# Kernel tuning notes

Hardware: AMD Instinct MI355X
Metric: run time of the kernel (lower is better)

## Reference

```python
import jax, jax.numpy as jnp
import numpy as np

C = 64          # channels
HEADS = 4       # num_heads -> head_dim = 16
HID = int(C * 2.66)  # 170, GDFN hidden channels
B, H, W = 2, 256, 256


def conv1x1(x, w):
    # x: (b,c,h,w), w: (o,c) -> pointwise conv, no bias
    return jnp.einsum('bchw,oc->bohw', x, w)


def dwconv3x3(x, w):
    # depthwise 3x3, SAME padding; w: (C,1,3,3)
    return jax.lax.conv_general_dilated(
        x, w, window_strides=(1, 1), padding='SAME',
        feature_group_count=x.shape[1],
        dimension_numbers=('NCHW', 'OIHW', 'NCHW'))


def layer_norm_c(x, w, b):
    # torch: LayerNorm over channel dim of (b, hw, c), eps=1e-5
    mu = x.mean(axis=1, keepdims=True)
    var = ((x - mu) ** 2).mean(axis=1, keepdims=True)
    xn = (x - mu) / jnp.sqrt(var + 1e-5)
    return xn * w[None, :, None, None] + b[None, :, None, None]


def l2norm(x):
    # F.normalize(dim=-1), eps=1e-12
    n = jnp.sqrt(jnp.sum(x * x, axis=-1, keepdims=True))
    return x / jnp.maximum(n, 1e-12)


def mdta(x, temp, w_qkv, w_qkv_dw, w_po, w_kv, w_kv_dw, w_pof):
    b, c, h, w_ = x.shape
    d = c // HEADS
    qkv = dwconv3x3(conv1x1(x, w_qkv), w_qkv_dw)
    q, k, v = jnp.split(qkv, 3, axis=1)
    rs = lambda t: t.reshape(b, HEADS, d, h * w_)
    q, k, v = l2norm(rs(q)), l2norm(rs(k)), rs(v)
    # channel attention: (b,heads,d,d), softmax over last dim
    attn = jax.nn.softmax(jnp.einsum('bhdn,bhen->bhde', q, k) * temp, axis=-1)
    out = conv1x1(jnp.einsum('bhde,bhen->bhdn', attn, v).reshape(b, c, h, w_), w_po)
    # second gated branch: kv from `out`, reuse attn (qf/kf/attnf are dead code in source)
    kvf = dwconv3x3(conv1x1(out, w_kv), w_kv_dw)
    _kf, vf = jnp.split(kvf, 2, axis=1)
    vf = rs(vf)
    outf = conv1x1(jnp.einsum('bhde,bhen->bhdn', attn, vf).reshape(b, c, h, w_), w_pof)
    return outf


def gdfn(x, w_in, w_dw, w_out):
    x12 = dwconv3x3(conv1x1(x, w_in), w_dw)
    x1, x2 = jnp.split(x12, 2, axis=1)
    return conv1x1(jax.nn.gelu(x1, approximate=False) * x2, w_out)


def setup_inputs() -> dict:
    key = jax.random.key(0)
    ks = jax.random.split(key, 10)
    s = 0.05
    return {
        'x': jax.random.normal(ks[0], (B, C, H, W), jnp.float32),
        'n1_w': jnp.ones((C,), jnp.float32),
        'n1_b': jnp.zeros((C,), jnp.float32),
        'temp': jnp.ones((1, HEADS, 1, 1), jnp.float32),
        'w_qkv': jax.random.normal(ks[1], (3 * C, C), jnp.float32) * s,
        'w_qkv_dw': jax.random.normal(ks[2], (3 * C, 1, 3, 3), jnp.float32) * s,
        'w_po': jax.random.normal(ks[3], (C, C), jnp.float32) * s,
        'w_kv': jax.random.normal(ks[4], (2 * C, C), jnp.float32) * s,
        'w_kv_dw': jax.random.normal(ks[5], (2 * C, 1, 3, 3), jnp.float32) * s,
        'w_pof': jax.random.normal(ks[6], (C, C), jnp.float32) * s,
        'n2_w': jnp.ones((C,), jnp.float32),
        'n2_b': jnp.zeros((C,), jnp.float32),
        'w_in': jax.random.normal(ks[7], (2 * HID, C), jnp.float32) * s,
        'w_dw': jax.random.normal(ks[8], (2 * HID, 1, 3, 3), jnp.float32) * s,
        'w_out': jax.random.normal(ks[9], (C, HID), jnp.float32) * s,
    }


def reference(x, n1_w, n1_b, temp, w_qkv, w_qkv_dw, w_po, w_kv, w_kv_dw, w_pof,
              n2_w, n2_b, w_in, w_dw, w_out):
    x = x + mdta(layer_norm_c(x, n1_w, n1_b), temp,
                 w_qkv, w_qkv_dw, w_po, w_kv, w_kv_dw, w_pof)
    x = x + gdfn(layer_norm_c(x, n2_w, n2_b), w_in, w_dw, w_out)
    return x
```

## Files before the change

kernel.cpp:

```cpp
#include <hip/hip_runtime.h>
#include <hip/hip_bf16.h>
#include <math.h>

#define NPB 65536
#define BATCH 2
#define NTOT (BATCH * NPB)

typedef unsigned short u16;
typedef __attribute__((ext_vector_type(8))) short short8;
typedef __attribute__((ext_vector_type(4))) short short4v;
typedef __attribute__((ext_vector_type(4))) float f32x4;


__device__ __forceinline__ float bf2f(u16 u) {
  union { unsigned u; float f; } v; v.u = ((unsigned)u) << 16; return v.f;
}
__device__ __forceinline__ u16 f2bf(float f) {
  union { float f; unsigned u; } v; v.f = f;
  unsigned r = v.u + 0x7FFFu + ((v.u >> 16) & 1u);
  return (u16)(r >> 16);
}
__device__ __forceinline__ unsigned pk2(float a, float b) {
  return (unsigned)f2bf(a) | ((unsigned)f2bf(b) << 16);
}
__device__ __forceinline__ f32x4 mm(short8 a, short8 b, f32x4 c) {
  return __builtin_amdgcn_mfma_f32_16x16x32_bf16(a, b, c, 0, 0, 0);
}
__device__ __forceinline__ short8 ldfrag(const u16* F, int frag, int l) {
  return *reinterpret_cast<const short8*>(F + ((size_t)frag * 64 + l) * 8);
}
__device__ __forceinline__ void st4(u16* p, f32x4 c) {
  uint2 v; v.x = pk2(c[0], c[1]); v.y = pk2(c[2], c[3]);
  *reinterpret_cast<uint2*>(p) = v;
}
__device__ __forceinline__ float gelu_t(float a) {
  const float z = 0.7978845608f * fmaf(0.044715f * a, a * a, a);
  const float e = __expf(2.f * z);
  const float th = 1.f - 2.f / (e + 1.f);
  return 0.5f * a * (1.f + th);
}

__global__ __launch_bounds__(64) void k_wprep(
    const float* __restrict__ wqkv, const float* __restrict__ win,
    const float* __restrict__ wout, u16* __restrict__ WQf,
    u16* __restrict__ WIf, u16* __restrict__ WOf)
{
  const int f = blockIdx.x;
  const int l = threadIdx.x;
  const int fr = l & 15, fq = l >> 4;
  short8 v;
  u16* dst;
  if (f < 24) {
    const int t = f >> 1, kh = f & 1;
    const int row = t * 16 + fr;
#pragma unroll
    for (int j = 0; j < 8; ++j)
      v[j] = (short)f2bf(wqkv[(size_t)row * 64 + kh * 32 + fq * 8 + j]);
    dst = WQf + ((size_t)f * 64 + l) * 8;
  } else if (f < 68) {
    const int fi = f - 24;
    const int g = fi >> 1, kh = fi & 1;
    const int half = g / 11, t = g % 11;
    const int col = half * 176 + t * 16 + fr;
    const int row = col < 170 ? col : (col < 176 ? -1 : (col < 346 ? col - 6 : -1));
#pragma unroll
    for (int j = 0; j < 8; ++j)
      v[j] = (row < 0) ? (short)0
             : (short)f2bf(win[(size_t)row * 64 + kh * 32 + fq * 8 + j]);
    dst = WIf + ((size_t)fi * 64 + l) * 8;
  } else {
    const int fi = f - 68;
    const int t = fi / 6, kh = fi % 6;
    const int row = t * 16 + fr;
#pragma unroll
    for (int j = 0; j < 8; ++j) {
      const int k = kh * 32 + fq * 8 + j;
      v[j] = (k < 170) ? (short)f2bf(wout[(size_t)row * 170 + k]) : (short)0;
    }
    dst = WOf + ((size_t)fi * 64 + l) * 8;
  }
  *reinterpret_cast<short8*>(dst) = v;
}

__global__ __launch_bounds__(256, 2) void g_lnqkv(
    const float* __restrict__ x, const float* __restrict__ n1w,
    const float* __restrict__ n1b, const u16* __restrict__ WQf,
    u16* __restrict__ qkvp)
{
  const int l = threadIdx.x & 63, fr = l & 15, fq = l >> 4;
  const int wv = blockIdx.x * 4 + (threadIdx.x >> 6);
  const int nw = gridDim.x * 4;
  short8 A[12][2];
#pragma unroll
  for (int t = 0; t < 12; ++t)
#pragma unroll
    for (int kh = 0; kh < 2; ++kh) A[t][kh] = ldfrag(WQf, t * 2 + kh, l);
  float w0[8], g0[8], w1[8], g1[8];
#pragma unroll
  for (int j = 0; j < 8; ++j) {
    w0[j] = n1w[fq * 8 + j];      g0[j] = n1b[fq * 8 + j];
    w1[j] = n1w[32 + fq * 8 + j]; g1[j] = n1b[32 + fq * 8 + j];
  }
  for (int tile = wv; tile < 8192; tile += nw) {
    const size_t n = (size_t)tile * 16 + fr;
    const int b = (int)(n >> 16);
    const int pix = (int)(n & 65535);
    const float* xb = x + ((size_t)b * 64) * NPB + pix;
    float v0[8], v1[8];
    float s = 0.f;
#pragma unroll
    for (int j = 0; j < 8; ++j) { v0[j] = xb[(size_t)(fq * 8 + j) * NPB]; s += v0[j]; }
#pragma unroll
    for (int j = 0; j < 8; ++j) { v1[j] = xb[(size_t)(32 + fq * 8 + j) * NPB]; s += v1[j]; }
    s += __shfl_xor(s, 16); s += __shfl_xor(s, 32);
    const float mu = s * (1.f / 64.f);
    float ss = 0.f;
#pragma unroll
    for (int j = 0; j < 8; ++j) { float d = v0[j] - mu; ss = fmaf(d, d, ss); }
#pragma unroll
    for (int j = 0; j < 8; ++j) { float d = v1[j] - mu; ss = fmaf(d, d, ss); }
    ss += __shfl_xor(ss, 16); ss += __shfl_xor(ss, 32);
    const float rstd = rsqrtf(ss * (1.f / 64.f) + 1e-5f);
    short8 b0, b1;
#pragma unroll
    for (int j = 0; j < 8; ++j) {
      b0[j] = (short)f2bf((v0[j] - mu) * rstd * w0[j] + g0[j]);
      b1[j] = (short)f2bf((v1[j] - mu) * rstd * w1[j] + g1[j]);
    }
    f32x4 c[12];
#pragma unroll
    for (int t = 0; t < 12; ++t) c[t] = f32x4{0.f, 0.f, 0.f, 0.f};
#pragma unroll
    for (int t = 0; t < 12; ++t) c[t] = mm(A[t][0], b0, c[t]);
#pragma unroll
    for (int t = 0; t < 12; ++t) c[t] = mm(A[t][1], b1, c[t]);
#pragma unroll
    for (int t = 0; t < 12; ++t)
      st4(qkvp + ((size_t)t * NTOT + n) * 16 + fq * 4, c[t]);
  }
}

template<int CH, int STRIP>
__global__ __launch_bounds__(256, 2) void k_dwr(
    const u16* __restrict__ in, u16* __restrict__ out,
    const float* __restrict__ wdw, int wofs)
{
  typedef short __attribute__((ext_vector_type(CH))) shortC;
  constexpr int LPP = 16 / CH;
  constexpr int NX  = 256 / LPP;
  constexpr int XC  = 256 / NX;
  const int t = threadIdx.x;
  const int sub = t % LPP, xi = t / LPP;
  const int q = blockIdx.x / XC, xc = blockIdx.x % XC;
  const int strip = blockIdx.y, b = blockIdx.z;
  const int x = xc * NX + xi;
  const int y0 = strip * STRIP;
  const int e0 = sub * CH;
  const int c0 = q * 16 + e0;

  const u16* pin = in + ((size_t)q * NTOT + (size_t)b * NPB) * 16 + e0;

  float w[9][CH];
#pragma unroll
  for (int ch = 0; ch < CH; ++ch) {
    const int row = wofs + c0 + ch;
#pragma unroll
    for (int tap = 0; tap < 9; ++tap)
      w[tap][ch] = wdw[(size_t)row * 9 + tap];
  }

  auto LD = [&](int yy, int xx) -> shortC {
    shortC v;
#pragma unroll
    for (int j = 0; j < CH; ++j) v[j] = 0;
    if ((unsigned)yy < 256u && (unsigned)xx < 256u)
      v = *reinterpret_cast<const shortC*>(pin + (size_t)(yy * 256 + xx) * 16);
    return v;
  };

  shortC r[3][3];
  r[0][0] = LD(y0 - 1, x - 1); r[0][1] = LD(y0 - 1, x); r[0][2] = LD(y0 - 1, x + 1);
  r[1][0] = LD(y0, x - 1);     r[1][1] = LD(y0, x);     r[1][2] = LD(y0, x + 1);

#pragma unroll 2
  for (int yy = 0; yy < STRIP; ++yy) {
    const int y = y0 + yy;
    r[2][0] = LD(y + 1, x - 1); r[2][1] = LD(y + 1, x); r[2][2] = LD(y + 1, x + 1);
    float acc[CH];
#pragma unroll
    for (int ch = 0; ch < CH; ++ch) acc[ch] = 0.f;
#pragma unroll
    for (int ky = 0; ky < 3; ++ky)
#pragma unroll
      for (int kx = 0; kx < 3; ++kx)
#pragma unroll
        for (int ch = 0; ch < CH; ++ch)
          acc[ch] = fmaf(w[ky * 3 + kx][ch], bf2f((u16)r[ky][kx][ch]), acc[ch]);
    u16* po = out + ((size_t)q * NTOT + (size_t)b * NPB +
                     (size_t)(y * 256 + x)) * 16 + e0;
    uint4 o;
    o.x = pk2(acc[0], acc[1]); o.y = pk2(acc[2], acc[3]);
    o.z = pk2(acc[4], acc[5]); o.w = pk2(acc[6], acc[7]);
    *reinterpret_cast<uint4*>(po) = o;
#pragma unroll
    for (int dx = 0; dx < 3; ++dx) { r[0][dx] = r[1][dx]; r[1][dx] = r[2][dx]; }
  }
}

__global__ __launch_bounds__(256, 2) void g_windwg(
    const u16* __restrict__ Y2, const u16* __restrict__ WIf,
    const float* __restrict__ wdw, u16* __restrict__ Hg)
{
  __shared__ __align__(16) u16 sy[336 * 72];
  __shared__ __align__(16) u16 sh[336 * 36];
  __shared__ __align__(16) u16 swt[2 * 9 * 176];
  const int t = threadIdx.x;
  const int tx0 = blockIdx.x * 16, ty0 = blockIdx.y * 16;
  const int b = blockIdx.z;
  const size_t bofs = (size_t)b * NPB;

  for (int i = t; i < 2 * 9 * 176; i += 256) {
    const int pl = i / (9 * 176);
    const int r = i % (9 * 176);
    const int tap = r / 176, c = r % 176;
    swt[i] = (c < 170) ? f2bf(wdw[((size_t)(pl * 170 + c)) * 9 + tap]) : (u16)0;
  }
  for (int idx = t; idx < 336; idx += 256) {
    const int py = idx / 18, px = idx % 18;
    const int gy = ty0 + py - 1, gx = tx0 + px - 1;
    const bool ok = (idx < 324) && ((unsigned)gy < 256u) && ((unsigned)gx < 256u);
#pragma unroll
    for (int cb = 0; cb < 4; ++cb) {
      short8 v0, v1;
      if (ok) {
        const u16* src = Y2 + ((size_t)cb * NTOT + bofs + (size_t)(gy * 256 + gx)) * 16;
        v0 = *reinterpret_cast<const short8*>(src);
        v1 = *reinterpret_cast<const short8*>(src + 8);
      } else {
#pragma unroll
        for (int j = 0; j < 8; ++j) { v0[j] = 0; v1[j] = 0; }
      }
      *reinterpret_cast<short8*>(&sy[idx * 72 + cb * 16]) = v0;
      *reinterpret_cast<short8*>(&sy[idx * 72 + cb * 16 + 8]) = v1;
    }
  }
  __syncthreads();

  const int w = t >> 6, l = t & 63, fr = l & 15, fq = l >> 4;
  const int sub = t & 3, colx = (t >> 2) & 15, rg = t >> 6;
  const int e0 = sub * 4;

  for (int q = 0; q < 11; ++q) {
    const short8 a10 = ldfrag(WIf, q * 2, l);
    const short8 a11 = ldfrag(WIf, q * 2 + 1, l);
    const short8 a20 = ldfrag(WIf, (11 + q) * 2, l);
    const short8 a21 = ldfrag(WIf, (11 + q) * 2 + 1, l);
    for (int i = w; i < 21; i += 4) {
      const u16* sp = &sy[(i * 16 + fr) * 72];
      const short8 b0 = *reinterpret_cast<const short8*>(sp + fq * 8);
      const short8 b1 = *reinterpret_cast<const short8*>(sp + 32 + fq * 8);
      f32x4 c1 = {0.f, 0.f, 0.f, 0.f}, c2 = {0.f, 0.f, 0.f, 0.f};
      c1 = mm(a10, b0, c1); c1 = mm(a11, b1, c1);
      c2 = mm(a20, b0, c2); c2 = mm(a21, b1, c2);
      u16* dp = &sh[(i * 16 + fr) * 36];
      st4(dp + fq * 4, c1);
      st4(dp + 16 + fq * 4, c2);
    }
    __syncthreads();

    float wf[2][9][4];
#pragma unroll
    for (int pl = 0; pl < 2; ++pl)
#pragma unroll
      for (int tap = 0; tap < 9; ++tap) {
        const short4v wv = *reinterpret_cast<const short4v*>(
            &swt[(pl * 9 + tap) * 176 + q * 16 + e0]);
#pragma unroll
        for (int j = 0; j < 4; ++j) wf[pl][tap][j] = bf2f((u16)wv[j]);
      }
    short4v rwin[3][3][2];
    auto LDR = [&](int hr, int slot) {
#pragma unroll
      for (int dx = 0; dx < 3; ++dx)
#pragma unroll
        for (int pl = 0; pl < 2; ++pl)
          rwin[slot][dx][pl] = *reinterpret_cast<const short4v*>(
              &sh[(hr * 18 + colx + dx) * 36 + pl * 16 + e0]);
    };
    const int r0 = rg * 4;
    LDR(r0, 0); LDR(r0 + 1, 1);
#pragma unroll
    for (int k = 0; k < 4; ++k) {
      LDR(r0 + k + 2, (k + 2) % 3);
      const int s0 = k % 3, s1 = (k + 1) % 3, s2 = (k + 2) % 3;
      float acc[2][4] = {{0.f, 0.f, 0.f, 0.f}, {0.f, 0.f, 0.f, 0.f}};
#pragma unroll
      for (int pl = 0; pl < 2; ++pl)
#pragma unroll
        for (int dx = 0; dx < 3; ++dx)
#pragma unroll
          for (int j = 0; j < 4; ++j) {
            acc[pl][j] = fmaf(wf[pl][0 + dx][j], bf2f((u16)rwin[s0][dx][pl][j]), acc[pl][j]);
            acc[pl][j] = fmaf(wf[pl][3 + dx][j], bf2f((u16)rwin[s1][dx][pl][j]), acc[pl][j]);
            acc[pl][j] = fmaf(wf[pl][6 + dx][j], bf2f((u16)rwin[s2][dx][pl][j]), acc[pl][j]);
          }
      float v[4];
#pragma unroll
      for (int j = 0; j < 4; ++j) v[j] = gelu_t(acc[0][j]) * acc[1][j];
      const int gy = ty0 + r0 + k, gx = tx0 + colx;
      uint2 o; o.x = pk2(v[0], v[1]); o.y = pk2(v[2], v[3]);
      *reinterpret_cast<uint2*>(
          Hg + ((size_t)q * NTOT + bofs + (size_t)(gy * 256 + gx)) * 16 + e0) = o;
    }
    __syncthreads();
  }
}

__global__ __launch_bounds__(256, 2) void k_gram_p(
    const u16* __restrict__ qkv, float* __restrict__ part)
{
  __shared__ __align__(16) u16 lds[32][520];
  const int chunk = blockIdx.x, h = blockIdx.y, b = blockIdx.z;
  const int t = threadIdx.x;
#pragma unroll
  for (int i = 0; i < 2; ++i) {
    const int p = t + i * 256;
    const size_t pix = (size_t)b * NPB + chunk * 512 + p;
    const u16* srcq = qkv + ((size_t)h * NTOT + pix) * 16;
    const u16* srck = qkv + ((size_t)(4 + h) * NTOT + pix) * 16;
    const short8 q0 = *reinterpret_cast<const short8*>(srcq);
    const short8 q1 = *reinterpret_cast<const short8*>(srcq + 8);
    const short8 k0 = *reinterpret_cast<const short8*>(srck);
    const short8 k1 = *reinterpret_cast<const short8*>(srck + 8);
#pragma unroll
    for (int j = 0; j < 8; ++j) {
      lds[j][p] = (u16)q0[j];  lds[8 + j][p] = (u16)q1[j];
      lds[16 + j][p] = (u16)k0[j]; lds[24 + j][p] = (u16)k1[j];
    }
  }
  __syncthreads();
  const int w = t >> 6, l = t & 63, fr = l & 15, fq = l >> 4;
  if (w >= 3) return;
  float* pp = part + ((size_t)((b * 4 + h) * 128) + chunk) * 288;
  const int rowA = (w == 2) ? 16 + fr : fr;
  const int rowB = (w == 0) ? 16 + fr : rowA;
  f32x4 acc = {0.f, 0.f, 0.f, 0.f};
#pragma unroll
  for (int kt = 0; kt < 16; ++kt) {
    const short8 a  = *reinterpret_cast<const short8*>(&lds[rowA][kt * 32 + fq * 8]);
    const short8 bb = *reinterpret_cast<const short8*>(&lds[rowB][kt * 32 + fq * 8]);
    acc = mm(a, bb, acc);
  }
  if (w == 0) {
#pragma unroll
    for (int r = 0; r < 4; ++r) pp[(fq * 4 + r) * 16 + fr] = acc[r];
  } else if ((fr >> 2) == fq) {
    pp[(w == 1 ? 256 : 272) + fr] = acc[fr & 3];
  }
}

__global__ __launch_bounds__(320) void k_gram_red(
    const float* __restrict__ part, float* __restrict__ G,
    float* __restrict__ Sq, float* __restrict__ Sk)
{
  const int bh = blockIdx.x;
  const int t = threadIdx.x;
  if (t >= 288) return;
  const float* p = part + (size_t)bh * 128 * 288 + t;
  float s = 0.f;
  for (int ch = 0; ch < 128; ++ch) s += p[(size_t)ch * 288];
  const int b = bh >> 2, h = bh & 3;
  if (t < 256) G[bh * 256 + t] = s;
  else if (t < 272) Sq[b * 64 + h * 16 + (t - 256)] = s;
  else Sk[b * 64 + h * 16 + (t - 272)] = s;
}

__global__ __launch_bounds__(256) void k_attn(
    const float* __restrict__ G, const float* __restrict__ Sq,
    const float* __restrict__ Sk, const float* __restrict__ temp,
    const float* __restrict__ wpo, const float* __restrict__ wkv,
    const float* __restrict__ wpof, u16* __restrict__ Pf,
    u16* __restrict__ M2f)
{
  __shared__ float attn[BATCH][4][16][16];
  __shared__ float M1[BATCH][64][64];
  __shared__ float rq[128], rk[128];
  const int t = threadIdx.x;
  if (t < 128) {
    rq[t] = 1.f / fmaxf(sqrtf(Sq[t]), 1e-12f);
    rk[t] = 1.f / fmaxf(sqrtf(Sk[t]), 1e-12f);
  }
  __syncthreads();
  if (t < 128) {
    const int b = t >> 6, h = (t >> 4) & 3, d = t & 15;
    const float tm = temp[h];
    const float* g = G + ((b * 4 + h) * 16 + d) * 16;
    const float rqd = rq[b * 64 + h * 16 + d];
    float L[16], mx = -1e30f;
#pragma unroll
    for (int e = 0; e < 16; ++e) {
      L[e] = g[e] * rqd * rk[b * 64 + h * 16 + e] * tm;
      mx = fmaxf(mx, L[e]);
    }
    float s = 0.f;
#pragma unroll
    for (int e = 0; e < 16; ++e) { L[e] = expf(L[e] - mx); s += L[e]; }
    const float inv = 1.f / s;
#pragma unroll
    for (int e = 0; e < 16; ++e) attn[b][h][d][e] = L[e] * inv;
  }
  __syncthreads();
  for (int s0 = 0; s0 < 32; ++s0) {
    const int idx = t * 32 + s0;
    const int b = idx >> 12, o = (idx >> 6) & 63, c = idx & 63;
    const int h = c >> 4, e = c & 15;
    float a = 0.f;
#pragma unroll
    for (int d = 0; d < 16; ++d) a = fmaf(wpo[o * 64 + h * 16 + d], attn[b][h][d][e], a);
    M1[b][o][c] = a;
  }
  __syncthreads();
  for (int it = 0; it < 4; ++it) {
    const int idx = it * 256 + t;
    const int l = idx & 63;
    const int fi = idx >> 6;
    const int b = fi >> 3, tt = (fi >> 1) & 3, kh = fi & 1;
    const int fr = l & 15, fq = l >> 4;
    const int o = tt * 16 + fr;
    short8 pv, mv;
#pragma unroll
    for (int j = 0; j < 8; ++j) {
      const int c = kh * 32 + fq * 8 + j;
      const int h = c >> 4, e = c & 15;
      float a2 = 0.f;
#pragma unroll
      for (int d = 0; d < 16; ++d)
        a2 = fmaf(wpof[o * 64 + h * 16 + d], attn[b][h][d][e], a2);
      mv[j] = (short)f2bf(a2);
      float a = 0.f;
      for (int jj = 0; jj < 64; ++jj)
        a = fmaf(wkv[(64 + o) * 64 + jj], M1[b][jj][c], a);
      pv[j] = (short)f2bf(a);
    }
    *reinterpret_cast<short8*>(Pf + ((size_t)fi * 64 + l) * 8) = pv;
    *reinterpret_cast<short8*>(M2f + ((size_t)fi * 64 + l) * 8) = mv;
  }
}

__global__ __launch_bounds__(256, 2) void g_pv(
    const u16* __restrict__ qkv, const u16* __restrict__ Pf,
    u16* __restrict__ vfp)
{
  const int l = threadIdx.x & 63, fr = l & 15, fq = l >> 4;
  const int wv = blockIdx.x * 4 + (threadIdx.x >> 6);
  const int nw = gridDim.x * 4;
  const int b = blockIdx.z;
  short8 A[4][2];
#pragma unroll
  for (int t = 0; t < 4; ++t)
#pragma unroll
    for (int kh = 0; kh < 2; ++kh)
      A[t][kh] = ldfrag(Pf, (b * 4 + t) * 2 + kh, l);
  const size_t hof = (size_t)(fq & 1) * 8;
  for (int tile = wv; tile < 4096; tile += nw) {
    const size_t n = (size_t)b * NPB + (size_t)tile * 16 + fr;
    const short8 b0 = *reinterpret_cast<const short8*>(
        qkv + ((size_t)(8 + (fq >> 1)) * NTOT + n) * 16 + hof);
    const short8 b1 = *reinterpret_cast<const short8*>(
        qkv + ((size_t)(10 + (fq >> 1)) * NTOT + n) * 16 + hof);
    f32x4 c[4];
#pragma unroll
    for (int t = 0; t < 4; ++t) c[t] = f32x4{0.f, 0.f, 0.f, 0.f};
#pragma unroll
    for (int t = 0; t < 4; ++t) c[t] = mm(A[t][0], b0, c[t]);
#pragma unroll
    for (int t = 0; t < 4; ++t) c[t] = mm(A[t][1], b1, c[t]);
#pragma unroll
    for (int t = 0; t < 4; ++t)
      st4(vfp + ((size_t)t * NTOT + n) * 16 + fq * 4, c[t]);
  }
}

__global__ __launch_bounds__(256, 2) void g_x2ln(
    const u16* __restrict__ vf, const u16* __restrict__ M2f,
    const float* __restrict__ x, const float* __restrict__ n2w,
    const float* __restrict__ n2b, u16* __restrict__ X2,
    u16* __restrict__ Y2)
{
  const int l = threadIdx.x & 63, fr = l & 15, fq = l >> 4;
  const int wv = blockIdx.x * 4 + (threadIdx.x >> 6);
  const int nw = gridDim.x * 4;
  const int b = blockIdx.z;
  short8 A[4][2];
#pragma unroll
  for (int t = 0; t < 4; ++t)
#pragma unroll
    for (int kh = 0; kh < 2; ++kh)
      A[t][kh] = ldfrag(M2f, (b * 4 + t) * 2 + kh, l);
  const size_t hof = (size_t)(fq & 1) * 8;
  for (int tile = wv; tile < 4096; tile += nw) {
    const int pix0 = tile * 16;
    const size_t n = (size_t)b * NPB + pix0 + fr;
    const short8 b0 = *reinterpret_cast<const short8*>(
        vf + ((size_t)(fq >> 1) * NTOT + n) * 16 + hof);
    const short8 b1 = *reinterpret_cast<const short8*>(
        vf + ((size_t)(2 + (fq >> 1)) * NTOT + n) * 16 + hof);
    f32x4 c[4];
#pragma unroll
    for (int t = 0; t < 4; ++t) c[t] = f32x4{0.f, 0.f, 0.f, 0.f};
#pragma unroll
    for (int t = 0; t < 4; ++t) c[t] = mm(A[t][0], b0, c[t]);
#pragma unroll
    for (int t = 0; t < 4; ++t) c[t] = mm(A[t][1], b1, c[t]);
    const int pix = pix0 + fr;
#pragma unroll
    for (int t = 0; t < 4; ++t)
#pragma unroll
      for (int r = 0; r < 4; ++r)
        c[t][r] += x[((size_t)(b * 64 + t * 16 + fq * 4 + r)) * NPB + pix];
#pragma unroll
    for (int t = 0; t < 4; ++t)
      st4(X2 + ((size_t)t * NTOT + n) * 16 + fq * 4, c[t]);
    float s = 0.f;
#pragma unroll
    for (int t = 0; t < 4; ++t)
#pragma unroll
      for (int r = 0; r < 4; ++r) s += c[t][r];
    s += __shfl_xor(s, 16); s += __shfl_xor(s, 32);
    const float mu = s * (1.f / 64.f);
    float ss = 0.f;
#pragma unroll
    for (int t = 0; t < 4; ++t)
#pragma unroll
      for (int r = 0; r < 4; ++r) { float d = c[t][r] - mu; ss = fmaf(d, d, ss); }
    ss += __shfl_xor(ss, 16); ss += __shfl_xor(ss, 32);
    const float rstd = rsqrtf(ss * (1.f / 64.f) + 1e-5f);
#pragma unroll
    for (int t = 0; t < 4; ++t)
#pragma unroll
      for (int r = 0; r < 4; ++r) {
        const int oc = t * 16 + fq * 4 + r;
        c[t][r] = (c[t][r] - mu) * rstd * n2w[oc] + n2b[oc];
      }
#pragma unroll
    for (int t = 0; t < 4; ++t)
      st4(Y2 + ((size_t)t * NTOT + n) * 16 + fq * 4, c[t]);
  }
}

__global__ __launch_bounds__(256, 2) void g_out(
    const u16* __restrict__ hg, const u16* __restrict__ WOf,
    const u16* __restrict__ X2, float* __restrict__ out)
{
  const int l = threadIdx.x & 63, fr = l & 15, fq = l >> 4;
  const int wv = blockIdx.x * 4 + (threadIdx.x >> 6);
  const int nw = gridDim.x * 4;
  short8 A[4][6];
#pragma unroll
  for (int t = 0; t < 4; ++t)
#pragma unroll
    for (int kh = 0; kh < 6; ++kh)
      A[t][kh] = ldfrag(WOf, t * 6 + kh, l);
  const size_t hof = (size_t)(fq & 1) * 8;
  for (int tile = wv; tile < 8192; tile += nw) {
    const size_t n = (size_t)tile * 16 + fr;
    short8 bb[6];
#pragma unroll
    for (int kh = 0; kh < 6; ++kh) {
      int hb = kh * 2 + (fq >> 1);
      if (hb > 10) hb = 10;
      bb[kh] = *reinterpret_cast<const short8*>(
          hg + ((size_t)hb * NTOT + n) * 16 + hof);
    }
    f32x4 c[4];
#pragma unroll
    for (int t = 0; t < 4; ++t) c[t] = f32x4{0.f, 0.f, 0.f, 0.f};
#pragma unroll
    for (int kh = 0; kh < 6; ++kh)
#pragma unroll
      for (int t = 0; t < 4; ++t) c[t] = mm(A[t][kh], bb[kh], c[t]);
    const int b = (int)(n >> 16);
    const int pix = (int)(n & 65535);
#pragma unroll
    for (int t = 0; t < 4; ++t) {
      const uint2 xv = *reinterpret_cast<const uint2*>(
          X2 + ((size_t)t * NTOT + n) * 16 + fq * 4);
      const u16 h0 = (u16)(xv.x & 0xffff), h1 = (u16)(xv.x >> 16);
      const u16 h2 = (u16)(xv.y & 0xffff), h3 = (u16)(xv.y >> 16);
      const int ocb = b * 64 + t * 16 + fq * 4;
      out[((size_t)(ocb + 0)) * NPB + pix] = c[t][0] + bf2f(h0);
      out[((size_t)(ocb + 1)) * NPB + pix] = c[t][1] + bf2f(h1);
      out[((size_t)(ocb + 2)) * NPB + pix] = c[t][2] + bf2f(h2);
      out[((size_t)(ocb + 3)) * NPB + pix] = c[t][3] + bf2f(h3);
    }
  }
}

extern "C" void kernel_launch(void* const* d_in, const int* in_sizes, int n_in,
                              void* d_out, int out_size, void* d_ws, size_t ws_size,
                              hipStream_t stream)
{
  const float* x     = (const float*)d_in[0];
  const float* n1w   = (const float*)d_in[1];
  const float* n1b   = (const float*)d_in[2];
  const float* temp  = (const float*)d_in[3];
  const float* wqkv  = (const float*)d_in[4];
  const float* wqkvd = (const float*)d_in[5];
  const float* wpo   = (const float*)d_in[6];
  const float* wkv   = (const float*)d_in[7];
  const float* wkvd  = (const float*)d_in[8];
  const float* wpof  = (const float*)d_in[9];
  const float* n2w   = (const float*)d_in[10];
  const float* n2b   = (const float*)d_in[11];
  const float* win   = (const float*)d_in[12];
  const float* wdw   = (const float*)d_in[13];
  const float* wout  = (const float*)d_in[14];
  float* out = (float*)d_out;

  char* ws = (char*)d_ws;
  const size_t offA  = 0;
  const size_t offB  = 16777216;
  const size_t offC  = offB + 50331648;
  const size_t offHg = offC + 50331648;
  const size_t offX2 = offHg + 46137344 + 256;
  const size_t offSm = offX2 + 16777216;

  u16* VFP  = (u16*)(ws + offA);
  u16* Y2   = (u16*)(ws + offA);
  u16* QKVp = (u16*)(ws + offB);
  u16* VF   = (u16*)(ws + offB);
  u16* QKV  = (u16*)(ws + offC);
  u16* Hg   = (u16*)(ws + offHg);
  u16* X2   = (u16*)(ws + offX2);
  float* part = (float*)(ws + offSm);
  float* G    = (float*)(ws + offSm + 1179648);
  float* Sq   = (float*)(ws + offSm + 1179648 + 8192);
  float* Sk   = (float*)(ws + offSm + 1179648 + 8704);
  u16* Pf     = (u16*)(ws + offSm + 1179648 + 9216);
  u16* M2f    = (u16*)(ws + offSm + 1179648 + 25600);
  u16* WQf    = (u16*)(ws + offSm + 1179648 + 41984);
  u16* WIf    = (u16*)(ws + offSm + 1179648 + 66560);
  u16* WOf    = (u16*)(ws + offSm + 1179648 + 111616);

  k_wprep<<<dim3(92), 64, 0, stream>>>(wqkv, win, wout, WQf, WIf, WOf);
  g_lnqkv<<<dim3(512), 256, 0, stream>>>(x, n1w, n1b, WQf, QKVp);
  k_dwr<8, 16><<<dim3(24, 16, BATCH), 256, 0, stream>>>(QKVp, QKV, wqkvd, 0);
  k_gram_p<<<dim3(128, 4, BATCH), 256, 0, stream>>>(QKV, part);
  k_gram_red<<<dim3(BATCH * 4), 320, 0, stream>>>(part, G, Sq, Sk);
  k_attn<<<dim3(1), 256, 0, stream>>>(G, Sq, Sk, temp, wpo, wkv, wpof, Pf, M2f);
  g_pv<<<dim3(256, 1, BATCH), 256, 0, stream>>>(QKV, Pf, VFP);
  k_dwr<8, 8><<<dim3(8, 32, BATCH), 256, 0, stream>>>(VFP, VF, wkvd, 64);
  g_x2ln<<<dim3(256, 1, BATCH), 256, 0, stream>>>(VF, M2f, x, n2w, n2b, X2, Y2);
  g_windwg<<<dim3(16, 16, BATCH), 256, 0, stream>>>(Y2, WIf, wdw, Hg);
  g_out<<<dim3(512), 256, 0, stream>>>(Hg, WOf, X2, out);
}
```

Measured before the change: 224.0 us.

## Fuse PV matmul with depthwise 3x3 conv into one tiled kernel

Replaces the separate PV MFMA kernel and the following depthwise 3x3 conv kernel with a single kernel. It computes the projected values for a 16x16 tile plus a one-pixel halo into shared memory, then applies the depthwise conv from LDS. This drops a full intermediate write and re-read of the VFP buffer in global memory and removes one launch. In exchange it recomputes the halo pixels (about 324/256 of the matmul work) and uses more shared memory per block, which may limit occupancy.

```diff
diff --git a/kernel.cpp b/kernel.cpp
--- a/kernel.cpp
+++ b/kernel.cpp
@@ -204,6 +204,100 @@
     *reinterpret_cast<uint4*>(po) = o;
 #pragma unroll
     for (int dx = 0; dx < 3; ++dx) { r[0][dx] = r[1][dx]; r[1][dx] = r[2][dx]; }
+  }
+}
+
+__global__ __launch_bounds__(256, 2) void g_pvdw(
+    const u16* __restrict__ QKV, const u16* __restrict__ Pf,
+    const float* __restrict__ wkvd, u16* __restrict__ VF)
+{
+  __shared__ __align__(16) u16 sh[336 * 68];
+  __shared__ __align__(16) u16 swt[9 * 64];
+  const int t = threadIdx.x;
+  const int tx0 = blockIdx.x * 16, ty0 = blockIdx.y * 16;
+  const int b = blockIdx.z;
+  const size_t bofs = (size_t)b * NPB;
+
+  for (int i = t; i < 9 * 64; i += 256) {
+    const int tap = i >> 6, c = i & 63;
+    swt[i] = f2bf(wkvd[((size_t)(64 + c)) * 9 + tap]);
+  }
+
+  const int w = t >> 6, l = t & 63, fr = l & 15, fq = l >> 4;
+  short8 A[4][2];
+#pragma unroll
+  for (int tt = 0; tt < 4; ++tt)
+#pragma unroll
+    for (int kh = 0; kh < 2; ++kh)
+      A[tt][kh] = ldfrag(Pf, (b * 4 + tt) * 2 + kh, l);
+  const size_t hof = (size_t)(fq & 1) * 8;
+
+  for (int i = w; i < 21; i += 4) {
+    const int hidx = i * 16 + fr;
+    const int hs = hidx < 323 ? hidx : 323;
+    const int py = hs / 18, px = hs % 18;
+    const int gy = ty0 + py - 1, gx = tx0 + px - 1;
+    const bool ok = ((unsigned)gy < 256u) && ((unsigned)gx < 256u);
+    short8 b0, b1;
+    if (ok) {
+      const size_t pix = bofs + (size_t)(gy * 256 + gx);
+      b0 = *reinterpret_cast<const short8*>(
+          QKV + ((size_t)(8 + (fq >> 1)) * NTOT + pix) * 16 + hof);
+      b1 = *reinterpret_cast<const short8*>(
+          QKV + ((size_t)(10 + (fq >> 1)) * NTOT + pix) * 16 + hof);
+    } else {
+#pragma unroll
+      for (int j = 0; j < 8; ++j) { b0[j] = 0; b1[j] = 0; }
+    }
+    f32x4 c[4];
+#pragma unroll
+    for (int tt = 0; tt < 4; ++tt) c[tt] = f32x4{0.f, 0.f, 0.f, 0.f};
+#pragma unroll
+    for (int tt = 0; tt < 4; ++tt) c[tt] = mm(A[tt][0], b0, c[tt]);
+#pragma unroll
+    for (int tt = 0; tt < 4; ++tt) c[tt] = mm(A[tt][1], b1, c[tt]);
+    u16* dp = &sh[hidx * 68];
+#pragma unroll
+    for (int tt = 0; tt < 4; ++tt) st4(dp + tt * 16 + fq * 4, c[tt]);
+  }
+  __syncthreads();
+
+  const int sub = t & 3, colx = (t >> 2) & 15, rg = t >> 6;
+  const int e0 = sub * 4;
+  for (int cb = 0; cb < 4; ++cb) {
+    float wf[9][4];
+#pragma unroll
+    for (int tap = 0; tap < 9; ++tap)
+#pragma unroll
+      for (int j = 0; j < 4; ++j)
+        wf[tap][j] = bf2f(swt[tap * 64 + cb * 16 + e0 + j]);
+    short4v rwin[3][3];
+    auto LDR = [&](int hr, int slot) {
+#pragma unroll
+      for (int dx = 0; dx < 3; ++dx)
+        rwin[slot][dx] = *reinterpret_cast<const short4v*>(
+            &sh[(hr * 18 + colx + dx) * 68 + cb * 16 + e0]);
+    };
+    const int r0 = rg * 4;
+    LDR(r0, 0); LDR(r0 + 1, 1);
+#pragma unroll
+    for (int k = 0; k < 4; ++k) {
+      LDR(r0 + k + 2, (k + 2) % 3);
+      const int s0 = k % 3, s1 = (k + 1) % 3, s2 = (k + 2) % 3;
+      float acc[4] = {0.f, 0.f, 0.f, 0.f};
+#pragma unroll
+      for (int dx = 0; dx < 3; ++dx)
+#pragma unroll
+        for (int j = 0; j < 4; ++j) {
+          acc[j] = fmaf(wf[0 + dx][j], bf2f((u16)rwin[s0][dx][j]), acc[j]);
+          acc[j] = fmaf(wf[3 + dx][j], bf2f((u16)rwin[s1][dx][j]), acc[j]);
+          acc[j] = fmaf(wf[6 + dx][j], bf2f((u16)rwin[s2][dx][j]), acc[j]);
+        }
+      const int gy = ty0 + r0 + k, gx = tx0 + colx;
+      uint2 o; o.x = pk2(acc[0], acc[1]); o.y = pk2(acc[2], acc[3]);
+      *reinterpret_cast<uint2*>(
+          VF + ((size_t)cb * NTOT + bofs + (size_t)(gy * 256 + gx)) * 16 + e0) = o;
+    }
   }
 }
 
@@ -444,40 +538,6 @@
     }
     *reinterpret_cast<short8*>(Pf + ((size_t)fi * 64 + l) * 8) = pv;
     *reinterpret_cast<short8*>(M2f + ((size_t)fi * 64 + l) * 8) = mv;
-  }
-}
-
-__global__ __launch_bounds__(256, 2) void g_pv(
-    const u16* __restrict__ qkv, const u16* __restrict__ Pf,
-    u16* __restrict__ vfp)
-{
-  const int l = threadIdx.x & 63, fr = l & 15, fq = l >> 4;
-  const int wv = blockIdx.x * 4 + (threadIdx.x >> 6);
-  const int nw = gridDim.x * 4;
-  const int b = blockIdx.z;
-  short8 A[4][2];
-#pragma unroll
-  for (int t = 0; t < 4; ++t)
-#pragma unroll
-    for (int kh = 0; kh < 2; ++kh)
-      A[t][kh] = ldfrag(Pf, (b * 4 + t) * 2 + kh, l);
-  const size_t hof = (size_t)(fq & 1) * 8;
-  for (int tile = wv; tile < 4096; tile += nw) {
-    const size_t n = (size_t)b * NPB + (size_t)tile * 16 + fr;
-    const short8 b0 = *reinterpret_cast<const short8*>(
-        qkv + ((size_t)(8 + (fq >> 1)) * NTOT + n) * 16 + hof);
-    const short8 b1 = *reinterpret_cast<const short8*>(
-        qkv + ((size_t)(10 + (fq >> 1)) * NTOT + n) * 16 + hof);
-    f32x4 c[4];
-#pragma unroll
-    for (int t = 0; t < 4; ++t) c[t] = f32x4{0.f, 0.f, 0.f, 0.f};
-#pragma unroll
-    for (int t = 0; t < 4; ++t) c[t] = mm(A[t][0], b0, c[t]);
-#pragma unroll
-    for (int t = 0; t < 4; ++t) c[t] = mm(A[t][1], b1, c[t]);
-#pragma unroll
-    for (int t = 0; t < 4; ++t)
-      st4(vfp + ((size_t)t * NTOT + n) * 16 + fq * 4, c[t]);
   }
 }
 
@@ -625,7 +685,6 @@
   const size_t offX2 = offHg + 46137344 + 256;
   const size_t offSm = offX2 + 16777216;
 
-  u16* VFP  = (u16*)(ws + offA);
   u16* Y2   = (u16*)(ws + offA);
   u16* QKVp = (u16*)(ws + offB);
   u16* VF   = (u16*)(ws + offB);
@@ -648,8 +707,7 @@
   k_gram_p<<<dim3(128, 4, BATCH), 256, 0, stream>>>(QKV, part);
   k_gram_red<<<dim3(BATCH * 4), 320, 0, stream>>>(part, G, Sq, Sk);
   k_attn<<<dim3(1), 256, 0, stream>>>(G, Sq, Sk, temp, wpo, wkv, wpof, Pf, M2f);
-  g_pv<<<dim3(256, 1, BATCH), 256, 0, stream>>>(QKV, Pf, VFP);
-  k_dwr<8, 8><<<dim3(8, 32, BATCH), 256, 0, stream>>>(VFP, VF, wkvd, 64);
+  g_pvdw<<<dim3(16, 16, BATCH), 256, 0, stream>>>(QKV, Pf, wkvd, VF);
   g_x2ln<<<dim3(256, 1, BATCH), 256, 0, stream>>>(VF, M2f, x, n2w, n2b, X2, Y2);
   g_windwg<<<dim3(16, 16, BATCH), 256, 0, stream>>>(Y2, WIf, wdw, Hg);
   g_out<<<dim3(512), 256, 0, stream>>>(Hg, WOf, X2, out);
```

Measured after the change: 218.3 us (median of 3 runs). 2.5% less time.
